# Kernel optimization log

Measured on AMD Instinct MI355X. Metric: run time of the kernel, lower is better.

## Reference

```python
import jax, jax.numpy as jnp
import numpy as np

N = 4096


def setup_inputs() -> dict:
    key = jax.random.key(0)
    ks = jax.random.split(key, 24)

    def idx(k, n, cols):
        base = jax.random.randint(k, (n,), 0, N)
        return jnp.stack([(base + j) % N for j in range(cols)], axis=1).astype(jnp.int32)

    x = jax.random.normal(ks[0], (N, 3), jnp.float32) * 3.0  # spread points so min pair dist is not tiny
    bond = idx(ks[1], 6144, 2)
    kb = jax.random.uniform(ks[2], (6144,), jnp.float32)
    b0 = jax.random.uniform(ks[3], (6144,), jnp.float32)
    angle = idx(ks[4], 8192, 3)
    kt = jax.random.uniform(ks[5], (8192,), jnp.float32)
    t0 = jax.random.uniform(ks[6], (8192,), jnp.float32) * 180.0  # degrees
    ureybradley = idx(ks[7], 4096, 2)
    ku = jax.random.uniform(ks[8], (4096,), jnp.float32)
    s0 = jax.random.uniform(ks[9], (4096,), jnp.float32)
    dihedral = idx(ks[10], 12288, 4)
    kd = jax.random.uniform(ks[11], (12288,), jnp.float32)
    nd = jax.random.randint(ks[12], (12288,), 1, 4).astype(jnp.float32)  # multiplicity
    d0 = jax.random.uniform(ks[13], (12288,), jnp.float32) * 360.0
    improper = idx(ks[14], 2048, 4)
    kp = jax.random.uniform(ks[15], (2048,), jnp.float32)
    p0 = jax.random.uniform(ks[16], (2048,), jnp.float32) * 180.0
    eps_ij = jax.random.uniform(ks[17], (N, N), jnp.float32)
    rmin_ij = jax.random.uniform(ks[18], (N, N), jnp.float32) * 0.5
    kqq_ij = jax.random.normal(ks[19], (N, N), jnp.float32)
    return dict(x=x, kb=kb, b0=b0, kt=kt, t0=t0, ku=ku, s0=s0, kd=kd, nd=nd, d0=d0,
                kp=kp, p0=p0, eps_ij=eps_ij, rmin_ij=rmin_ij, kqq_ij=kqq_ij,
                bond=bond, angle=angle, ureybradley=ureybradley,
                dihedral=dihedral, improper=improper, central=0)


def _torsion(x, quad):
    # signed dihedral angle for [M,4] index quadruples
    ab = x[quad[:, 1]] - x[quad[:, 0]]
    bc = x[quad[:, 2]] - x[quad[:, 1]]
    cd = x[quad[:, 3]] - x[quad[:, 2]]
    n1 = jnp.cross(ab, bc)
    n2 = jnp.cross(bc, cd)
    cos_d = jnp.sum(n1 * n2, axis=1) / (jnp.linalg.norm(n1, axis=1) * jnp.linalg.norm(n2, axis=1))
    ang = jnp.arccos(jnp.clip(cos_d, -0.9999, 0.9999))
    return ang * jnp.sign(jnp.sum(jnp.cross(n1, n2) * bc, axis=1))


def _energy(x, kb, b0, kt, t0, ku, s0, kd, nd, d0, kp, p0,
            eps_ij, rmin_ij, kqq_ij, bond, angle, ureybradley, dihedral, improper, central):
    # bonds
    dis = jnp.linalg.norm(x[bond[:, 0]] - x[bond[:, 1]], axis=1)
    V_bond = jnp.sum(kb * (dis - b0) ** 2)
    # angles
    ba = x[angle[:, 0]] - x[angle[:, 1]]
    bc = x[angle[:, 2]] - x[angle[:, 1]]
    cos_t = jnp.sum(ba * bc, axis=1) / (jnp.linalg.norm(ba, axis=1) * jnp.linalg.norm(bc, axis=1))
    theta = jnp.arccos(jnp.clip(cos_t, -0.9999, 0.9999))
    V_angle = jnp.sum(kt * (theta - jnp.deg2rad(t0)) ** 2)
    # Urey-Bradley 1-3 terms
    dub = jnp.linalg.norm(x[ureybradley[:, 0]] - x[ureybradley[:, 1]], axis=1)
    V_ub = jnp.sum(ku * (dub - s0) ** 2)
    # proper dihedrals
    delta = _torsion(x, dihedral)
    V_dih = jnp.sum(kd * (1.0 + jnp.cos(nd * delta - jnp.deg2rad(d0))))
    # impropers (harmonic)
    psi = _torsion(x, improper)
    V_imp = jnp.sum(kp * (psi - jnp.deg2rad(p0)) ** 2)
    # nonbonded: cdist(x,x) + I, summed over strict upper triangle
    n = x.shape[0]
    sq = jnp.sum(x * x, axis=1)
    d2 = jnp.maximum(sq[:, None] + sq[None, :] - 2.0 * (x @ x.T), 1e-12)
    eye = jnp.eye(n, dtype=bool)
    dist = jnp.sqrt(jnp.where(eye, 1.0, d2))  # diag -> 1, matching cdist + eye
    rod = rmin_ij / dist
    vdw = eps_ij * (rod ** 12 - 2.0 * rod ** 6)
    mask = jnp.triu(jnp.ones((n, n), bool), 1)
    V_vdw = jnp.sum(jnp.where(mask, vdw, 0.0))
    V_ele = jnp.sum(jnp.where(mask, kqq_ij / dist, 0.0))
    V = V_bond + V_angle + V_ub + V_dih + V_imp + V_vdw + V_ele
    if central:
        V = V + jnp.sum(0.1 * jnp.sum((x - jnp.mean(x, axis=0)) ** 2, axis=1))
    return V


def reference(x, kb, b0, kt, t0, ku, s0, kd, nd, d0, kp, p0,
              eps_ij, rmin_ij, kqq_ij, bond, angle, ureybradley, dihedral, improper, central):
    return _energy(x, kb, b0, kt, t0, ku, s0, kd, nd, d0, kp, p0,
                   eps_ij, rmin_ij, kqq_ij, bond, angle, ureybradley, dihedral, improper, central)
```

## Files before the change

kernel.cpp:

```cpp
#include <hip/hip_runtime.h>

#define NATOM   4096
#define NG4     (NATOM / 4)
#define NBOND   6144
#define NANGLE  8192
#define NUB     4096
#define NDIH    12288
#define NIMP    2048

#define NB_BLOCKS   2048
#define BOND_ITEMS  (NBOND + NANGLE + NUB + NDIH + NIMP)
#define ITEMS_PER_BLOCK (BOND_ITEMS / NB_BLOCKS)
#define TOTAL_SLOTS NB_BLOCKS

#define DEG2RAD 0.017453292519943295f

static __device__ __forceinline__ double block_reduce(double v, double* sm) {
    #pragma unroll
    for (int off = 32; off > 0; off >>= 1) v += __shfl_down(v, off, 64);
    const int lane = threadIdx.x & 63, wid = threadIdx.x >> 6;
    __syncthreads();
    if (lane == 0) sm[wid] = v;
    __syncthreads();
    double r = 0.0;
    if (threadIdx.x == 0) {
        const int nw = blockDim.x >> 6;
        for (int w = 0; w < nw; ++w) r += sm[w];
    }
    return r;
}

static __device__ __forceinline__ float pair_term(
    float xi0, float xi1, float xi2,
    float xj0, float xj1, float xj2,
    float e, float r, float q, bool valid)
{
    const float dx = xi0 - xj0, dy = xi1 - xj1, dz = xi2 - xj2;
    float d2 = fmaf(dx, dx, fmaf(dy, dy, dz * dz));
    d2 = fmaxf(d2, 1e-12f);
    float inv = rsqrtf(d2);
    const float t = inv * inv;
    inv = inv * fmaf(-0.5f * d2, t, 1.5f);
    const float rod = r * inv;
    const float r2 = rod * rod;
    const float r6 = r2 * r2 * r2;
    const float v = fmaf(e * r6, r6 - 2.0f, q * inv);
    return valid ? v : 0.0f;
}

static __device__ __forceinline__ float group_term(
    int i, float xi0, float xi1, float xi2, int g,
    float4 e, float4 r, float4 q, float4 xa, float4 xb, float4 xc)
{
    const int j0 = 4 * g;
    float s;
    s  = pair_term(xi0,xi1,xi2, xa.x,xa.y,xa.z, e.x,r.x,q.x, j0+0 > i);
    s += pair_term(xi0,xi1,xi2, xa.w,xb.x,xb.y, e.y,r.y,q.y, j0+1 > i);
    s += pair_term(xi0,xi1,xi2, xb.z,xb.w,xc.x, e.z,r.z,q.z, j0+2 > i);
    s += pair_term(xi0,xi1,xi2, xc.y,xc.z,xc.w, e.w,r.w,q.w, j0+3 > i);
    return s;
}

static __device__ __forceinline__ float torsion(const float* __restrict__ x,
                                                int i0, int i1, int i2, int i3) {
    const float ax = x[3*i1] - x[3*i0], ay = x[3*i1+1] - x[3*i0+1], az = x[3*i1+2] - x[3*i0+2];
    const float bx = x[3*i2] - x[3*i1], by = x[3*i2+1] - x[3*i1+1], bz = x[3*i2+2] - x[3*i1+2];
    const float cx = x[3*i3] - x[3*i2], cy = x[3*i3+1] - x[3*i2+1], cz = x[3*i3+2] - x[3*i2+2];
    const float n1x = ay*bz - az*by, n1y = az*bx - ax*bz, n1z = ax*by - ay*bx;
    const float n2x = by*cz - bz*cy, n2y = bz*cx - bx*cz, n2z = bx*cy - by*cx;
    const float dt  = n1x*n2x + n1y*n2y + n1z*n2z;
    const float nn1 = sqrtf(n1x*n1x + n1y*n1y + n1z*n1z);
    const float nn2 = sqrtf(n2x*n2x + n2y*n2y + n2z*n2z);
    float c = dt / (nn1 * nn2);
    c = fminf(fmaxf(c, -0.9999f), 0.9999f);
    const float ang = acosf(c);
    const float sx = n1y*n2z - n1z*n2y, sy = n1z*n2x - n1x*n2z, sz = n1x*n2y - n1y*n2x;
    const float s = sx*bx + sy*by + sz*bz;
    const float sg = (s > 0.0f) ? 1.0f : ((s < 0.0f) ? -1.0f : 0.0f);
    return ang * sg;
}

static __device__ __forceinline__ float bonded_item(
    const float* __restrict__ x, int t,
    const float* __restrict__ kb, const float* __restrict__ b0,
    const float* __restrict__ kt, const float* __restrict__ t0,
    const float* __restrict__ ku, const float* __restrict__ s0,
    const float* __restrict__ kd, const float* __restrict__ nd, const float* __restrict__ d0,
    const float* __restrict__ kp, const float* __restrict__ p0,
    const int* __restrict__ bond, const int* __restrict__ angle,
    const int* __restrict__ ub,   const int* __restrict__ dih,
    const int* __restrict__ imp)
{
    if (t < NBOND) {
        const int m = t;
        const int i = bond[2*m], j = bond[2*m+1];
        const float dx = x[3*i]-x[3*j], dy = x[3*i+1]-x[3*j+1], dz = x[3*i+2]-x[3*j+2];
        const float dis = sqrtf(dx*dx + dy*dy + dz*dz);
        const float d = dis - b0[m];
        return kb[m] * d * d;
    } else if (t < NBOND + NANGLE) {
        const int m = t - NBOND;
        const int i = angle[3*m], j = angle[3*m+1], k = angle[3*m+2];
        const float bax = x[3*i]-x[3*j], bay = x[3*i+1]-x[3*j+1], baz = x[3*i+2]-x[3*j+2];
        const float bcx = x[3*k]-x[3*j], bcy = x[3*k+1]-x[3*j+1], bcz = x[3*k+2]-x[3*j+2];
        const float dt  = bax*bcx + bay*bcy + baz*bcz;
        const float na  = sqrtf(bax*bax + bay*bay + baz*baz);
        const float nb  = sqrtf(bcx*bcx + bcy*bcy + bcz*bcz);
        float c = dt / (na * nb);
        c = fminf(fmaxf(c, -0.9999f), 0.9999f);
        const float theta = acosf(c);
        const float d = theta - t0[m] * DEG2RAD;
        return kt[m] * d * d;
    } else if (t < NBOND + NANGLE + NUB) {
        const int m = t - NBOND - NANGLE;
        const int i = ub[2*m], j = ub[2*m+1];
        const float dx = x[3*i]-x[3*j], dy = x[3*i+1]-x[3*j+1], dz = x[3*i+2]-x[3*j+2];
        const float dis = sqrtf(dx*dx + dy*dy + dz*dz);
        const float d = dis - s0[m];
        return ku[m] * d * d;
    } else if (t < NBOND + NANGLE + NUB + NDIH) {
        const int m = t - NBOND - NANGLE - NUB;
        const float delta = torsion(x, dih[4*m], dih[4*m+1], dih[4*m+2], dih[4*m+3]);
        return kd[m] * (1.0f + cosf(nd[m] * delta - d0[m] * DEG2RAD));
    } else {
        const int m = t - NBOND - NANGLE - NUB - NDIH;
        const float psi = torsion(x, imp[4*m], imp[4*m+1], imp[4*m+2], imp[4*m+3]);
        const float d = psi - p0[m] * DEG2RAD;
        return kp[m] * d * d;
    }
}

__global__ __launch_bounds__(256) void ff_kernel(
    const float4* __restrict__ xv,
    const float4* __restrict__ eps,
    const float4* __restrict__ rmin,
    const float4* __restrict__ kqq,
    const float* __restrict__ kb, const float* __restrict__ b0,
    const float* __restrict__ kt, const float* __restrict__ t0,
    const float* __restrict__ ku, const float* __restrict__ s0,
    const float* __restrict__ kd, const float* __restrict__ nd, const float* __restrict__ d0,
    const float* __restrict__ kp, const float* __restrict__ p0,
    const int* __restrict__ bond, const int* __restrict__ angle,
    const int* __restrict__ ub,   const int* __restrict__ dih,
    const int* __restrict__ imp,  const int* __restrict__ central,
    double* __restrict__ ws)
{
    __shared__ double sm[4];
    const float* __restrict__ x = (const float*)xv;
    const int b = (int)blockIdx.x;
    const int t = (int)threadIdx.x;

    const int i0 = b, i1 = NATOM - 1 - b;
    const int g00 = (i0 + 1) >> 2;
    const int g01 = (i1 + 1) >> 2;
    const int c0  = NG4 - g00;
    const int c1  = NG4 - g01;
    const int S   = c0 + c1;

    const float a0x = x[3*i0], a0y = x[3*i0+1], a0z = x[3*i0+2];
    const float a1x = x[3*i1], a1y = x[3*i1+1], a1z = x[3*i1+2];

    int   gs[4], is[4], idx[4];
    float xs0[4], xs1[4], xs2[4];
    #pragma unroll
    for (int u = 0; u < 4; ++u) {
        const int s   = t + (u << 8);
        const bool in0 = s < c0;
        const int g   = in0 ? (g00 + s) : (g01 + (s - c0));
        gs[u]  = g;
        is[u]  = in0 ? i0 : i1;
        xs0[u] = in0 ? a0x : a1x;
        xs1[u] = in0 ? a0y : a1y;
        xs2[u] = in0 ? a0z : a1z;
        idx[u] = (in0 ? i0 : i1) * NG4 + g;
    }

    float4 le[4], lr[4], lq[4];
    #pragma unroll
    for (int u = 0; u < 4; ++u) le[u] = eps [idx[u]];
    #pragma unroll
    for (int u = 0; u < 4; ++u) lr[u] = rmin[idx[u]];
    #pragma unroll
    for (int u = 0; u < 4; ++u) lq[u] = kqq [idx[u]];

    double acc = 0.0;
    #pragma unroll
    for (int u = 0; u < 4; ++u) {
        const int g3 = 3 * gs[u];
        const float4 xa = xv[g3], xb = xv[g3+1], xc = xv[g3+2];
        acc += (double)group_term(is[u], xs0[u], xs1[u], xs2[u], gs[u],
                                  le[u], lr[u], lq[u], xa, xb, xc);
    }

    if (S > 1024) {
        if (t == 0) {
            const int g  = g01 + (1024 - c0);
            const int id = i1 * NG4 + g;
            const float4 e = eps[id], r = rmin[id], q = kqq[id];
            const int g3 = 3 * g;
            const float4 xa = xv[g3], xb = xv[g3+1], xc = xv[g3+2];
            acc += (double)group_term(i1, a1x, a1y, a1z, g, e, r, q, xa, xb, xc);
        }
    }

    if (t < ITEMS_PER_BLOCK) {
        const int item = b * ITEMS_PER_BLOCK + t;
        acc += (double)bonded_item(x, item, kb, b0, kt, t0, ku, s0,
                                   kd, nd, d0, kp, p0, bond, angle, ub, dih, imp);
    }

    double cext = 0.0;
    if (b == 0) {
        if (*central != 0) {
            double sx = 0.0, sy = 0.0, sz = 0.0, s2 = 0.0;
            for (int i = t; i < NATOM; i += 256) {
                const float px = x[3*i], py = x[3*i+1], pz = x[3*i+2];
                sx += px; sy += py; sz += pz;
                s2 += (double)px*px + (double)py*py + (double)pz*pz;
            }
            const double rx = block_reduce(sx, sm);
            const double ry = block_reduce(sy, sm);
            const double rz = block_reduce(sz, sm);
            const double r2 = block_reduce(s2, sm);
            if (t == 0)
                cext = 0.1 * (r2 - (rx*rx + ry*ry + rz*rz) / (double)NATOM);
        }
    }

    const double tot = block_reduce(acc, sm);
    if (t == 0) ws[b] = tot + cext;
}

__global__ __launch_bounds__(256) void finalize_kernel(const double* __restrict__ ws,
                                                       float* __restrict__ out) {
    __shared__ double sm[4];
    double v = 0.0;
    for (int i = threadIdx.x; i < TOTAL_SLOTS; i += 256) v += ws[i];
    const double tot = block_reduce(v, sm);
    if (threadIdx.x == 0) out[0] = (float)tot;
}

extern "C" void kernel_launch(void* const* d_in, const int* in_sizes, int n_in,
                              void* d_out, int out_size, void* d_ws, size_t ws_size,
                              hipStream_t stream) {
    const float* x    = (const float*)d_in[0];
    const float* kb   = (const float*)d_in[1];
    const float* b0   = (const float*)d_in[2];
    const float* kt   = (const float*)d_in[3];
    const float* t0   = (const float*)d_in[4];
    const float* ku   = (const float*)d_in[5];
    const float* s0   = (const float*)d_in[6];
    const float* kd   = (const float*)d_in[7];
    const float* nd   = (const float*)d_in[8];
    const float* d0   = (const float*)d_in[9];
    const float* kp   = (const float*)d_in[10];
    const float* p0   = (const float*)d_in[11];
    const float* eps  = (const float*)d_in[12];
    const float* rmin = (const float*)d_in[13];
    const float* kqq  = (const float*)d_in[14];
    const int* bond   = (const int*)d_in[15];
    const int* angle  = (const int*)d_in[16];
    const int* ub     = (const int*)d_in[17];
    const int* dih    = (const int*)d_in[18];
    const int* imp    = (const int*)d_in[19];
    const int* cent   = (const int*)d_in[20];

    double* ws = (double*)d_ws;

    ff_kernel<<<NB_BLOCKS, 256, 0, stream>>>(
        (const float4*)x, (const float4*)eps, (const float4*)rmin, (const float4*)kqq,
        kb, b0, kt, t0, ku, s0, kd, nd, d0, kp, p0,
        bond, angle, ub, dih, imp, cent, ws);
    finalize_kernel<<<1, 256, 0, stream>>>(ws, (float*)d_out);
}
```

Baseline: 216.9 us.

## Stream pair matrices through LDS with double-buffered async global_load_lds

Replaces the register-held batch of eps/rmin/kqq float4 loads with async global-to-LDS loads into a two-stage shared-memory ring. Each of the four chunks is prefetched one step ahead, guarded by manual vmcnt waits and barriers. The aim is to overlap memory latency with the pair-term compute and reduce register pressure. It adds barriers per chunk, and the hand-written vmcnt counts depend on exact load ordering, which is fragile because the xv loads also count toward vmcnt.

```diff
diff --git a/kernel.cpp b/kernel.cpp
--- a/kernel.cpp
+++ b/kernel.cpp
@@ -14,6 +14,11 @@
 #define TOTAL_SLOTS NB_BLOCKS
 
 #define DEG2RAD 0.017453292519943295f
+
+#define GLOAD16(g, l)                                                     \
+    __builtin_amdgcn_global_load_lds(                                     \
+        (__attribute__((address_space(1))) void*)(g),                     \
+        (__attribute__((address_space(3))) void*)(l), 16, 0, 0)
 
 static __device__ __forceinline__ double block_reduce(double v, double* sm) {
     #pragma unroll
@@ -145,10 +150,12 @@
     const int* __restrict__ imp,  const int* __restrict__ central,
     double* __restrict__ ws)
 {
+    __shared__ float4 bufE[2][256], bufR[2][256], bufQ[2][256];
     __shared__ double sm[4];
     const float* __restrict__ x = (const float*)xv;
     const int b = (int)blockIdx.x;
     const int t = (int)threadIdx.x;
+    const int lane = t & 63, w = t >> 6;
 
     const int i0 = b, i1 = NATOM - 1 - b;
     const int g00 = (i0 + 1) >> 2;
@@ -160,36 +167,46 @@
     const float a0x = x[3*i0], a0y = x[3*i0+1], a0z = x[3*i0+2];
     const float a1x = x[3*i1], a1y = x[3*i1+1], a1z = x[3*i1+2];
 
-    int   gs[4], is[4], idx[4];
-    float xs0[4], xs1[4], xs2[4];
-    #pragma unroll
-    for (int u = 0; u < 4; ++u) {
-        const int s   = t + (u << 8);
+    auto stage = [&](int c, int bi) {
+        const int s   = (c << 8) + (w << 6) + lane;
         const bool in0 = s < c0;
         const int g   = in0 ? (g00 + s) : (g01 + (s - c0));
-        gs[u]  = g;
-        is[u]  = in0 ? i0 : i1;
-        xs0[u] = in0 ? a0x : a1x;
-        xs1[u] = in0 ? a0y : a1y;
-        xs2[u] = in0 ? a0z : a1z;
-        idx[u] = (in0 ? i0 : i1) * NG4 + g;
-    }
-
-    float4 le[4], lr[4], lq[4];
+        const int id  = (in0 ? i0 : i1) * NG4 + g;
+        float4* bE = &bufE[bi][w << 6];
+        float4* bR = &bufR[bi][w << 6];
+        float4* bQ = &bufQ[bi][w << 6];
+        GLOAD16(eps  + id, bE);
+        GLOAD16(rmin + id, bR);
+        GLOAD16(kqq  + id, bQ);
+    };
+
+    double acc = 0.0;
+
+    stage(0, 0);
     #pragma unroll
-    for (int u = 0; u < 4; ++u) le[u] = eps [idx[u]];
-    #pragma unroll
-    for (int u = 0; u < 4; ++u) lr[u] = rmin[idx[u]];
-    #pragma unroll
-    for (int u = 0; u < 4; ++u) lq[u] = kqq [idx[u]];
-
-    double acc = 0.0;
-    #pragma unroll
-    for (int u = 0; u < 4; ++u) {
-        const int g3 = 3 * gs[u];
+    for (int c = 0; c < 4; ++c) {
+        if (c < 3) {
+            stage(c + 1, (c + 1) & 1);
+            asm volatile("s_waitcnt vmcnt(3)" ::: "memory");
+        } else {
+            asm volatile("s_waitcnt vmcnt(0)" ::: "memory");
+        }
+        __builtin_amdgcn_s_barrier();
+        __builtin_amdgcn_sched_barrier(0);
+
+        const int s   = (c << 8) + t;
+        const bool in0 = s < c0;
+        const int g   = in0 ? (g00 + s) : (g01 + (s - c0));
+        const int bi  = c & 1;
+        const float4 e = bufE[bi][t], r = bufR[bi][t], q = bufQ[bi][t];
+        const int g3 = 3 * g;
         const float4 xa = xv[g3], xb = xv[g3+1], xc = xv[g3+2];
-        acc += (double)group_term(is[u], xs0[u], xs1[u], xs2[u], gs[u],
-                                  le[u], lr[u], lq[u], xa, xb, xc);
+        acc += (double)group_term(in0 ? i0 : i1,
+                                  in0 ? a0x : a1x, in0 ? a0y : a1y, in0 ? a0z : a1z,
+                                  g, e, r, q, xa, xb, xc);
+
+        __builtin_amdgcn_sched_barrier(0);
+        __builtin_amdgcn_s_barrier();
     }
 
     if (S > 1024) {
```

Result: no change. 213.6 us (-1.5%).
